# Performance work log

Hardware: AMD Instinct MI355X
Metric: run time of the kernel (lower is better)

## Reference

```python
import jax, jax.numpy as jnp
import numpy as np

NEG = -1e30  # log(0) surrogate that stays finite in fp32
BLANK = 0


def setup_inputs() -> dict:
    key = jax.random.key(0)
    k1, k2 = jax.random.split(key)
    B, T, V, L = 32, 1024, 1024, 256
    logits = jax.random.normal(k1, (B, T, V), dtype=jnp.float32)
    log_probs = jax.nn.log_softmax(logits, axis=-1)  # module expects log-probs
    labels = jax.random.randint(k2, (B, L), 1, V, dtype=jnp.int32)  # avoid blank=0
    input_lens = jnp.full((B,), T, dtype=jnp.int32)
    label_lens = jnp.full((B,), L, dtype=jnp.int32)
    return {"log_probs": log_probs, "labels": labels,
            "input_lens": input_lens, "label_lens": label_lens}


def _ctc_loss_sum(log_probs, labels, input_lens, label_lens, blank=BLANK):
    """CTC forward DP (alpha recursion) in log space; reduction='sum', zero_infinity=True."""
    B, T, V = log_probs.shape
    L = labels.shape[1]
    S = 2 * L + 1  # extended label: blank l1 blank l2 ... blank

    ext = jnp.full((B, S), blank, dtype=labels.dtype)
    ext = ext.at[:, 1::2].set(labels)
    # skip transition s-2 -> s allowed iff ext[s] != blank and ext[s] != ext[s-2]
    skip = jnp.concatenate(
        [jnp.zeros((B, 2), dtype=bool),
         (ext[:, 2:] != blank) & (ext[:, 2:] != ext[:, :-2])], axis=1)

    lp_tbv = jnp.transpose(log_probs, (1, 0, 2))  # 'btv->tbv' as in the module

    emit0 = jnp.take_along_axis(lp_tbv[0], ext, axis=1)  # [B,S]
    alpha0 = jnp.full((B, S), NEG, dtype=log_probs.dtype)
    alpha0 = alpha0.at[:, 0].set(emit0[:, 0]).at[:, 1].set(emit0[:, 1])

    neg1 = jnp.full((B, 1), NEG, dtype=log_probs.dtype)
    neg2 = jnp.full((B, 2), NEG, dtype=log_probs.dtype)

    def step(alpha, inputs):
        lp_t, t = inputs  # lp_t: [B,V]
        em = jnp.take_along_axis(lp_t, ext, axis=1)  # [B,S]
        a1 = alpha
        a2 = jnp.concatenate([neg1, alpha[:, :-1]], axis=1)
        a3 = jnp.where(skip, jnp.concatenate([neg2, alpha[:, :-2]], axis=1), NEG)
        new = jnp.logaddexp(jnp.logaddexp(a1, a2), a3) + em
        # freeze alpha once past this sample's input length
        new = jnp.where((t < input_lens)[:, None], new, alpha)
        return new, None

    ts = jnp.arange(1, T)
    alpha, _ = jax.lax.scan(step, alpha0, (lp_tbv[1:], ts))

    s_last = 2 * label_lens  # final blank state index per sample
    a_last = jnp.take_along_axis(alpha, s_last[:, None], axis=1)[:, 0]
    a_prev = jnp.take_along_axis(alpha, (s_last - 1)[:, None], axis=1)[:, 0]
    loss_b = -jnp.logaddexp(a_last, a_prev)
    loss_b = jnp.where(loss_b > 1e29, 0.0, loss_b)  # zero_infinity=True
    return jnp.sum(loss_b)


def reference(log_probs, labels, input_lens, label_lens):
    return _ctc_loss_sum(log_probs, labels, input_lens, label_lens)
```

## Files before the change

### kernel.cpp

```cpp
#include <hip/hip_runtime.h>


constexpr int B_ = 32, T_ = 1024, V_ = 1024, L_ = 256;
constexpr int S_ = 2 * L_ + 1;
constexpr int CH = 16;
constexpr int NCHUNK = 64;
constexpr int NBUF = 4;
constexpr float LN2F = 0.6931471805599453f;

typedef const __attribute__((address_space(1))) unsigned int* gp_t;
typedef __attribute__((address_space(3))) unsigned int* lp_t;

template <int CTRL>
__device__ __forceinline__ float dpp_fmax(float x) {
    const int t = __builtin_amdgcn_update_dpp(0, __float_as_int(x), CTRL, 0xf, 0xf, true);
    return fmaxf(x, __int_as_float(t));
}

__device__ __forceinline__ float wave_max_dpp(float x) {
    x = dpp_fmax<0x111>(x);
    x = dpp_fmax<0x112>(x);
    x = dpp_fmax<0x114>(x);
    x = dpp_fmax<0x118>(x);
    x = dpp_fmax<0x142>(x);
    x = dpp_fmax<0x143>(x);
    return __int_as_float(__builtin_amdgcn_readlane(__float_as_int(x), 63));
}

__device__ __forceinline__ float dpp_wave_shr1(float x) {
    return __int_as_float(
        __builtin_amdgcn_update_dpp(0, __float_as_int(x), 0x138, 0xf, 0xf, true));
}

__global__ __launch_bounds__(256, 8) void ctc_gather(
    float* __restrict__ lp, const int* __restrict__ labels,
    float* __restrict__ blanks)
{
    __shared__ float srow[4][V_];
    const int wave = threadIdx.x >> 6;
    const int lane = threadIdx.x & 63;
    const int r = blockIdx.x * 4 + wave;
    const int b = r >> 10;
    float* row = lp + (size_t)r * V_;
    const int* labb = labels + b * L_;

    #pragma unroll
    for (int j = 0; j < 4; ++j)
        __builtin_amdgcn_global_load_lds((gp_t)(row + 256 * j + 4 * lane),
                                         (lp_t)&srow[wave][256 * j], 16, 0, 0);
    const int4 e = *(const int4*)(labb + 4 * lane);
    asm volatile("s_waitcnt vmcnt(0)" ::: "memory");
    __builtin_amdgcn_sched_barrier(0);
    const float v0 = srow[wave][e.x];
    const float v1 = srow[wave][e.y];
    const float v2 = srow[wave][e.z];
    const float v3 = srow[wave][e.w];
    const float vb = srow[wave][0];
    float4 q;
    q.x = __expf(v0); q.y = __expf(v1); q.z = __expf(v2); q.w = __expf(v3);
    const float qb = __expf(vb);
    *(float4*)(row + 4 * lane) = q;
    if (lane == 0) {
        const int t = r & (T_ - 1);
        blanks[(r & ~(T_ - 1)) + ((t + T_ - 1) & (T_ - 1))] = qb;
    }
}

__global__ __launch_bounds__(128, 1) void ctc_dp(
    const float* __restrict__ Q, const float* __restrict__ blanks,
    const int* __restrict__ labels, const int* __restrict__ input_lens,
    const int* __restrict__ label_lens, float* __restrict__ out)
{
    __shared__ float blk[T_ + 4];
    __shared__ float buf[NBUF][CH][256];
    __shared__ int Pf, Cf;
    const int b    = blockIdx.x;
    const int tid  = threadIdx.x;
    const int lane = tid & 63;
    const int wv   = tid >> 6;
    const float* Qb  = Q + (size_t)b * T_ * V_;
    const float* blg = blanks + b * T_;
    const int*  labb = labels + b * L_;
    const int il = input_lens[b];
    const int ll = label_lens[b];
    const int tend = il < T_ ? il : T_;

    if (tid == 0) { Pf = 0; Cf = 0; }
    __syncthreads();

    if (wv == 1) {
        #pragma unroll
        for (int i = 0; i < 4; ++i)
            __builtin_amdgcn_global_load_lds((gp_t)(blg + 256 * i + 4 * lane),
                                             (lp_t)&blk[256 * i], 16, 0, 0);
        #pragma unroll
        for (int i = 0; i < CH; ++i) {
            int t = 1 + i; if (t > T_ - 1) t = T_ - 1;
            __builtin_amdgcn_global_load_lds(
                (gp_t)(Qb + (size_t)t * V_ + 4 * lane),
                (lp_t)&buf[0][i][0], 16, 0, 0);
        }
        for (int c = 0; c < NCHUNK; ++c) {
            if (c + 1 < NCHUNK) {
                while (__hip_atomic_load(&Cf, __ATOMIC_ACQUIRE,
                                         __HIP_MEMORY_SCOPE_WORKGROUP) < c + 2 - NBUF) {}
                const int cb = (c + 1) & (NBUF - 1);
                #pragma unroll
                for (int i = 0; i < CH; ++i) {
                    int t = 1 + (c + 1) * CH + i; if (t > T_ - 1) t = T_ - 1;
                    __builtin_amdgcn_global_load_lds(
                        (gp_t)(Qb + (size_t)t * V_ + 4 * lane),
                        (lp_t)&buf[cb][i][0], 16, 0, 0);
                }
                asm volatile("s_waitcnt vmcnt(16)" ::: "memory");
            } else {
                asm volatile("s_waitcnt vmcnt(0)" ::: "memory");
            }
            if (lane == 0)
                __hip_atomic_store(&Pf, c + 1, __ATOMIC_RELEASE,
                                   __HIP_MEMORY_SCOPE_WORKGROUP);
        }
    } else {
        const int4 e  = *(const int4*)(labb + 4 * lane);
        const int  ep = (lane > 0) ? labb[4 * lane - 1] : -1;
        const float kf0 = ((8 * lane + 1) >= 3 && e.x != ep) ? 1.f : 0.f;
        const float kf1 = (e.y != e.x) ? 1.f : 0.f;
        const float kf2 = (e.z != e.y) ? 1.f : 0.f;
        const float kf3 = (e.w != e.z) ? 1.f : 0.f;
        const float bl0 = blg[T_ - 1];
        const float q00 = Qb[0];
        float p0 = (lane == 0) ? bl0 : 0.f;
        float p1 = (lane == 0) ? q00 : 0.f;
        float p2 = 0.f, p3 = 0.f, p4 = 0.f, p5 = 0.f,
              p6 = 0.f, p7 = 0.f, p8 = 0.f;
        int Esc = 0;
        float pm1 = 0.f;
        float sfP = 1.f, sfM = 1.f;

        auto snap = [&]() -> float {
            float m = fmaxf(fmaxf(fmaxf(fmaxf(p0, p1), fmaxf(p2, p3)),
                                  fmaxf(fmaxf(p4, p5), fmaxf(p6, p7))), p8);
            m = wave_max_dpp(m);
            const unsigned eb = (__float_as_uint(m) >> 23) & 0xffu;
            if (eb >= 1u && eb <= 254u) {
                unsigned k = 318u - eb;
                if (k > 254u) k = 254u;
                Esc += (int)k - 127;
                return __uint_as_float(k << 23);
            }
            return 1.f;
        };

        for (int c = 0; c < NCHUNK; ++c) {
            while (__hip_atomic_load(&Pf, __ATOMIC_ACQUIRE,
                                     __HIP_MEMORY_SCOPE_WORKGROUP) <= c) {}
            const float* base = &buf[c & (NBUF - 1)][0][0] + 4 * lane;
            float4 qv[CH];
            #pragma unroll
            for (int i = 0; i < CH; ++i)
                qv[i] = *(const float4*)(base + 256 * i);
            float bb[CH];
            #pragma unroll
            for (int i = 0; i < CH; i += 4) {
                const float4 t4 = *(const float4*)&blk[c * CH + i];
                bb[i] = t4.x; bb[i + 1] = t4.y;
                bb[i + 2] = t4.z; bb[i + 3] = t4.w;
            }
            #pragma unroll
            for (int i = 0; i < CH; ++i) {
                float4 q = qv[i];
                float qb = bb[i];
                if (i == 0) { q.x *= sfP; q.y *= sfP; q.z *= sfP; q.w *= sfP; qb *= sfP; }
                if (i == 8) { q.x *= sfM; q.y *= sfM; q.z *= sfM; q.w *= sfM; qb *= sfM; }
                const int t = 1 + c * CH + i;
                if (t < tend) {
                    const float n7 = fmaf(kf3, p5, p7 + p6) * q.w;
                    const float n8 = (p8 + p7) * qb;
                    const float pm1n = dpp_wave_shr1(n7);
                    const float n0 = (p0 + pm1) * qb;
                    const float n1 = fmaf(kf0, pm1, p1 + p0) * q.x;
                    const float n2 = (p2 + p1) * qb;
                    const float n3 = fmaf(kf1, p1, p3 + p2) * q.y;
                    const float n4 = (p4 + p3) * qb;
                    const float n5 = fmaf(kf2, p3, p5 + p4) * q.z;
                    const float n6 = (p6 + p5) * qb;
                    p0 = n0; p1 = n1; p2 = n2; p3 = n3; p4 = n4;
                    p5 = n5; p6 = n6; p7 = n7; p8 = n8; pm1 = pm1n;
                }
                if (i == 4)  sfM = snap();
                if (i == 12) sfP = snap();
            }
            if (lane == 0)
                __hip_atomic_store(&Cf, c + 1, __ATOMIC_RELEASE,
                                   __HIP_MEMORY_SCOPE_WORKGROUP);
        }
        p0 *= sfP; p1 *= sfP; p2 *= sfP; p3 *= sfP; p4 *= sfP;
        p5 *= sfP; p6 *= sfP; p7 *= sfP; p8 *= sfP;

        const int sl = 2 * ll;
        auto pick = [&](int s) -> float {
            if (s == 512) return __shfl(p8, 63);
            const int r = s & 7;
            float v = p0;
            v = (r == 1) ? p1 : v; v = (r == 2) ? p2 : v;
            v = (r == 3) ? p3 : v; v = (r == 4) ? p4 : v;
            v = (r == 5) ? p5 : v; v = (r == 6) ? p6 : v;
            v = (r == 7) ? p7 : v;
            return __shfl(v, s >> 3);
        };
        const float la = pick(sl);
        const float lb = pick(sl - 1);
        if (lane == 0) {
            const float tot = la + lb;
            float loss = (float)Esc * LN2F - __logf(tot);
            if (!(loss <= 1e29f)) loss = 0.f;
            atomicAdd(out, loss);
        }
    }
}

extern "C" void kernel_launch(void* const* d_in, const int* in_sizes, int n_in,
                              void* d_out, int out_size, void* d_ws, size_t ws_size,
                              hipStream_t stream) {
    float*       lp     = (float*)d_in[0];
    const int*   labels = (const int*)d_in[1];
    const int*   il     = (const int*)d_in[2];
    const int*   ll     = (const int*)d_in[3];
    float* out    = (float*)d_out;
    float* blanks = (float*)d_ws;

    hipMemsetAsync(out, 0, sizeof(float), stream);
    ctc_gather<<<dim3(B_ * T_ / 4), dim3(256), 0, stream>>>(lp, labels, blanks);
    ctc_dp<<<dim3(B_), dim3(128), 0, stream>>>(lp, blanks, labels, il, ll, out);
}
```

Measured before the change: 295.3 us.

## Replace producer/consumer LDS pipeline with single-wave register double-buffering and compact Q

```diff
diff --git a/kernel.cpp b/kernel.cpp
--- a/kernel.cpp
+++ b/kernel.cpp
@@ -2,10 +2,8 @@
 
 
 constexpr int B_ = 32, T_ = 1024, V_ = 1024, L_ = 256;
-constexpr int S_ = 2 * L_ + 1;
 constexpr int CH = 16;
 constexpr int NCHUNK = 64;
-constexpr int NBUF = 4;
 constexpr float LN2F = 0.6931471805599453f;
 
 typedef const __attribute__((address_space(1))) unsigned int* gp_t;
@@ -33,15 +31,16 @@
 }
 
 __global__ __launch_bounds__(256, 8) void ctc_gather(
-    float* __restrict__ lp, const int* __restrict__ labels,
-    float* __restrict__ blanks)
+    const float* __restrict__ lp, float* __restrict__ qdst, int qstride,
+    const int* __restrict__ labels, float* __restrict__ blanks)
 {
     __shared__ float srow[4][V_];
     const int wave = threadIdx.x >> 6;
     const int lane = threadIdx.x & 63;
     const int r = blockIdx.x * 4 + wave;
     const int b = r >> 10;
-    float* row = lp + (size_t)r * V_;
+    const float* row = lp + (size_t)r * V_;
+    float* orow = qdst + (size_t)r * qstride;
     const int* labb = labels + b * L_;
 
     #pragma unroll
@@ -59,163 +58,160 @@
     float4 q;
     q.x = __expf(v0); q.y = __expf(v1); q.z = __expf(v2); q.w = __expf(v3);
     const float qb = __expf(vb);
-    *(float4*)(row + 4 * lane) = q;
+    *(float4*)(orow + 4 * lane) = q;
     if (lane == 0) {
         const int t = r & (T_ - 1);
         blanks[(r & ~(T_ - 1)) + ((t + T_ - 1) & (T_ - 1))] = qb;
     }
 }
 
-__global__ __launch_bounds__(128, 1) void ctc_dp(
-    const float* __restrict__ Q, const float* __restrict__ blanks,
-    const int* __restrict__ labels, const int* __restrict__ input_lens,
-    const int* __restrict__ label_lens, float* __restrict__ out)
+__global__ __launch_bounds__(64, 1) void ctc_dp(
+    const float* __restrict__ Q, int qstride,
+    const float* __restrict__ blanks, const int* __restrict__ labels,
+    const int* __restrict__ input_lens, const int* __restrict__ label_lens,
+    float* __restrict__ out)
 {
-    __shared__ float blk[T_ + 4];
-    __shared__ float buf[NBUF][CH][256];
-    __shared__ int Pf, Cf;
+    __shared__ float blk[T_];
     const int b    = blockIdx.x;
-    const int tid  = threadIdx.x;
-    const int lane = tid & 63;
-    const int wv   = tid >> 6;
-    const float* Qb  = Q + (size_t)b * T_ * V_;
+    const int lane = threadIdx.x & 63;
+    const float* Qb  = Q + (size_t)b * T_ * qstride;
     const float* blg = blanks + b * T_;
     const int*  labb = labels + b * L_;
     const int il = input_lens[b];
     const int ll = label_lens[b];
     const int tend = il < T_ ? il : T_;
 
-    if (tid == 0) { Pf = 0; Cf = 0; }
-    __syncthreads();
-
-    if (wv == 1) {
-        #pragma unroll
-        for (int i = 0; i < 4; ++i)
-            __builtin_amdgcn_global_load_lds((gp_t)(blg + 256 * i + 4 * lane),
-                                             (lp_t)&blk[256 * i], 16, 0, 0);
+    #pragma unroll
+    for (int i = 0; i < 4; ++i)
+        __builtin_amdgcn_global_load_lds((gp_t)(blg + 256 * i + 4 * lane),
+                                         (lp_t)&blk[256 * i], 16, 0, 0);
+
+    const int4 e  = *(const int4*)(labb + 4 * lane);
+    const int  ep = (lane > 0) ? labb[4 * lane - 1] : -1;
+    const float kf0 = ((8 * lane + 1) >= 3 && e.x != ep) ? 1.f : 0.f;
+    const float kf1 = (e.y != e.x) ? 1.f : 0.f;
+    const float kf2 = (e.z != e.y) ? 1.f : 0.f;
+    const float kf3 = (e.w != e.z) ? 1.f : 0.f;
+    const float bl0 = blg[T_ - 1];
+    const float q00 = Qb[0];
+    float p0 = (lane == 0) ? bl0 : 0.f;
+    float p1 = (lane == 0) ? q00 : 0.f;
+    float p2 = 0.f, p3 = 0.f, p4 = 0.f, p5 = 0.f,
+          p6 = 0.f, p7 = 0.f, p8 = 0.f;
+    int Esc = 0;
+    float pm1 = 0.f;
+    float sfP = 1.f, sfM = 1.f;
+
+    asm volatile("s_waitcnt vmcnt(0)" ::: "memory");
+    __builtin_amdgcn_sched_barrier(0);
+
+    auto snap = [&]() -> float {
+        float m = fmaxf(fmaxf(fmaxf(fmaxf(p0, p1), fmaxf(p2, p3)),
+                              fmaxf(fmaxf(p4, p5), fmaxf(p6, p7))), p8);
+        m = wave_max_dpp(m);
+        const unsigned eb = (__float_as_uint(m) >> 23) & 0xffu;
+        if (eb >= 1u && eb <= 254u) {
+            unsigned k = 318u - eb;
+            if (k > 254u) k = 254u;
+            Esc += (int)k - 127;
+            return __uint_as_float(k << 23);
+        }
+        return 1.f;
+    };
+
+    auto qaddr = [&](int t) -> const float4* {
+        return (const float4*)(Qb + (size_t)t * qstride + 4 * lane);
+    };
+
+    float4 qa[CH], qbf[CH];
+    float4 bbA[4], bbB[4];
+    #pragma unroll
+    for (int i = 0; i < CH; ++i) { int t = 1 + i; qa[i] = *qaddr(t); }
+    #pragma unroll
+    for (int i = 0; i < CH; ++i) {
+        int t = 1 + CH + i; if (t > T_ - 1) t = T_ - 1;
+        qbf[i] = *qaddr(t);
+    }
+    #pragma unroll
+    for (int j = 0; j < 4; ++j) bbA[j] = *(const float4*)&blk[4 * j];
+    #pragma unroll
+    for (int j = 0; j < 4; ++j) bbB[j] = *(const float4*)&blk[CH + 4 * j];
+
+    auto compute_chunk = [&](int c, float4 (&qv)[CH], float4 (&bv)[4]) {
         #pragma unroll
         for (int i = 0; i < CH; ++i) {
-            int t = 1 + i; if (t > T_ - 1) t = T_ - 1;
-            __builtin_amdgcn_global_load_lds(
-                (gp_t)(Qb + (size_t)t * V_ + 4 * lane),
-                (lp_t)&buf[0][i][0], 16, 0, 0);
-        }
-        for (int c = 0; c < NCHUNK; ++c) {
-            if (c + 1 < NCHUNK) {
-                while (__hip_atomic_load(&Cf, __ATOMIC_ACQUIRE,
-                                         __HIP_MEMORY_SCOPE_WORKGROUP) < c + 2 - NBUF) {}
-                const int cb = (c + 1) & (NBUF - 1);
-                #pragma unroll
-                for (int i = 0; i < CH; ++i) {
-                    int t = 1 + (c + 1) * CH + i; if (t > T_ - 1) t = T_ - 1;
-                    __builtin_amdgcn_global_load_lds(
-                        (gp_t)(Qb + (size_t)t * V_ + 4 * lane),
-                        (lp_t)&buf[cb][i][0], 16, 0, 0);
-                }
-                asm volatile("s_waitcnt vmcnt(16)" ::: "memory");
-            } else {
-                asm volatile("s_waitcnt vmcnt(0)" ::: "memory");
+            float4 q = qv[i];
+            const int g = i & 3;
+            const float4 f4 = bv[i >> 2];
+            float qb = (g == 0) ? f4.x : (g == 1) ? f4.y
+                     : (g == 2) ? f4.z : f4.w;
+            if (i == 0) { q.x *= sfP; q.y *= sfP; q.z *= sfP; q.w *= sfP; qb *= sfP; }
+            if (i == 8) { q.x *= sfM; q.y *= sfM; q.z *= sfM; q.w *= sfM; qb *= sfM; }
+            const int t = 1 + c * CH + i;
+            if (t < tend) {
+                const float n7 = fmaf(kf3, p5, p7 + p6) * q.w;
+                const float n8 = (p8 + p7) * qb;
+                const float pm1n = dpp_wave_shr1(n7);
+                const float n0 = (p0 + pm1) * qb;
+                const float n1 = fmaf(kf0, pm1, p1 + p0) * q.x;
+                const float n2 = (p2 + p1) * qb;
+                const float n3 = fmaf(kf1, p1, p3 + p2) * q.y;
+                const float n4 = (p4 + p3) * qb;
+                const float n5 = fmaf(kf2, p3, p5 + p4) * q.z;
+                const float n6 = (p6 + p5) * qb;
+                p0 = n0; p1 = n1; p2 = n2; p3 = n3; p4 = n4;
+                p5 = n5; p6 = n6; p7 = n7; p8 = n8; pm1 = pm1n;
             }
-            if (lane == 0)
-                __hip_atomic_store(&Pf, c + 1, __ATOMIC_RELEASE,
-                                   __HIP_MEMORY_SCOPE_WORKGROUP);
-        }
-    } else {
-        const int4 e  = *(const int4*)(labb + 4 * lane);
-        const int  ep = (lane > 0) ? labb[4 * lane - 1] : -1;
-        const float kf0 = ((8 * lane + 1) >= 3 && e.x != ep) ? 1.f : 0.f;
-        const float kf1 = (e.y != e.x) ? 1.f : 0.f;
-        const float kf2 = (e.z != e.y) ? 1.f : 0.f;
-        const float kf3 = (e.w != e.z) ? 1.f : 0.f;
-        const float bl0 = blg[T_ - 1];
-        const float q00 = Qb[0];
-        float p0 = (lane == 0) ? bl0 : 0.f;
-        float p1 = (lane == 0) ? q00 : 0.f;
-        float p2 = 0.f, p3 = 0.f, p4 = 0.f, p5 = 0.f,
-              p6 = 0.f, p7 = 0.f, p8 = 0.f;
-        int Esc = 0;
-        float pm1 = 0.f;
-        float sfP = 1.f, sfM = 1.f;
-
-        auto snap = [&]() -> float {
-            float m = fmaxf(fmaxf(fmaxf(fmaxf(p0, p1), fmaxf(p2, p3)),
-                                  fmaxf(fmaxf(p4, p5), fmaxf(p6, p7))), p8);
-            m = wave_max_dpp(m);
-            const unsigned eb = (__float_as_uint(m) >> 23) & 0xffu;
-            if (eb >= 1u && eb <= 254u) {
-                unsigned k = 318u - eb;
-                if (k > 254u) k = 254u;
-                Esc += (int)k - 127;
-                return __uint_as_float(k << 23);
+            if (i == 4)  sfM = snap();
+            if (i == 12) sfP = snap();
+        }
+    };
+
+    for (int c = 0; c < NCHUNK; c += 2) {
+        compute_chunk(c, qa, bbA);
+        if (c + 2 < NCHUNK) {
+            #pragma unroll
+            for (int i = 0; i < CH; ++i) {
+                int t = 1 + (c + 2) * CH + i; if (t > T_ - 1) t = T_ - 1;
+                qa[i] = *qaddr(t);
             }
-            return 1.f;
-        };
-
-        for (int c = 0; c < NCHUNK; ++c) {
-            while (__hip_atomic_load(&Pf, __ATOMIC_ACQUIRE,
-                                     __HIP_MEMORY_SCOPE_WORKGROUP) <= c) {}
-            const float* base = &buf[c & (NBUF - 1)][0][0] + 4 * lane;
-            float4 qv[CH];
-            #pragma unroll
-            for (int i = 0; i < CH; ++i)
-                qv[i] = *(const float4*)(base + 256 * i);
-            float bb[CH];
-            #pragma unroll
-            for (int i = 0; i < CH; i += 4) {
-                const float4 t4 = *(const float4*)&blk[c * CH + i];
-                bb[i] = t4.x; bb[i + 1] = t4.y;
-                bb[i + 2] = t4.z; bb[i + 3] = t4.w;
+            #pragma unroll
+            for (int j = 0; j < 4; ++j)
+                bbA[j] = *(const float4*)&blk[(c + 2) * CH + 4 * j];
+        }
+        compute_chunk(c + 1, qbf, bbB);
+        if (c + 3 < NCHUNK) {
+            #pragma unroll
+            for (int i = 0; i < CH; ++i) {
+                int t = 1 + (c + 3) * CH + i; if (t > T_ - 1) t = T_ - 1;
+                qbf[i] = *qaddr(t);
             }
             #pragma unroll
-            for (int i = 0; i < CH; ++i) {
-                float4 q = qv[i];
-                float qb = bb[i];
-                if (i == 0) { q.x *= sfP; q.y *= sfP; q.z *= sfP; q.w *= sfP; qb *= sfP; }
-                if (i == 8) { q.x *= sfM; q.y *= sfM; q.z *= sfM; q.w *= sfM; qb *= sfM; }
-                const int t = 1 + c * CH + i;
-                if (t < tend) {
-                    const float n7 = fmaf(kf3, p5, p7 + p6) * q.w;
-                    const float n8 = (p8 + p7) * qb;
-                    const float pm1n = dpp_wave_shr1(n7);
-                    const float n0 = (p0 + pm1) * qb;
-                    const float n1 = fmaf(kf0, pm1, p1 + p0) * q.x;
-                    const float n2 = (p2 + p1) * qb;
-                    const float n3 = fmaf(kf1, p1, p3 + p2) * q.y;
-                    const float n4 = (p4 + p3) * qb;
-                    const float n5 = fmaf(kf2, p3, p5 + p4) * q.z;
-                    const float n6 = (p6 + p5) * qb;
-                    p0 = n0; p1 = n1; p2 = n2; p3 = n3; p4 = n4;
-                    p5 = n5; p6 = n6; p7 = n7; p8 = n8; pm1 = pm1n;
-                }
-                if (i == 4)  sfM = snap();
-                if (i == 12) sfP = snap();
-            }
-            if (lane == 0)
-                __hip_atomic_store(&Cf, c + 1, __ATOMIC_RELEASE,
-                                   __HIP_MEMORY_SCOPE_WORKGROUP);
-        }
-        p0 *= sfP; p1 *= sfP; p2 *= sfP; p3 *= sfP; p4 *= sfP;
-        p5 *= sfP; p6 *= sfP; p7 *= sfP; p8 *= sfP;
-
-        const int sl = 2 * ll;
-        auto pick = [&](int s) -> float {
-            if (s == 512) return __shfl(p8, 63);
-            const int r = s & 7;
-            float v = p0;
-            v = (r == 1) ? p1 : v; v = (r == 2) ? p2 : v;
-            v = (r == 3) ? p3 : v; v = (r == 4) ? p4 : v;
-            v = (r == 5) ? p5 : v; v = (r == 6) ? p6 : v;
-            v = (r == 7) ? p7 : v;
-            return __shfl(v, s >> 3);
-        };
-        const float la = pick(sl);
-        const float lb = pick(sl - 1);
-        if (lane == 0) {
-            const float tot = la + lb;
-            float loss = (float)Esc * LN2F - __logf(tot);
-            if (!(loss <= 1e29f)) loss = 0.f;
-            atomicAdd(out, loss);
-        }
+            for (int j = 0; j < 4; ++j)
+                bbB[j] = *(const float4*)&blk[(c + 3) * CH + 4 * j];
+        }
+    }
+    p0 *= sfP; p1 *= sfP; p2 *= sfP; p3 *= sfP; p4 *= sfP;
+    p5 *= sfP; p6 *= sfP; p7 *= sfP; p8 *= sfP;
+
+    const int sl = 2 * ll;
+    auto pick = [&](int s) -> float {
+        if (s == 512) return __shfl(p8, 63);
+        const int r = s & 7;
+        float v = p0;
+        v = (r == 1) ? p1 : v; v = (r == 2) ? p2 : v;
+        v = (r == 3) ? p3 : v; v = (r == 4) ? p4 : v;
+        v = (r == 5) ? p5 : v; v = (r == 6) ? p6 : v;
+        v = (r == 7) ? p7 : v;
+        return __shfl(v, s >> 3);
+    };
+    const float la = pick(sl);
+    const float lb = pick(sl - 1);
+    if (lane == 0) {
+        const float tot = la + lb;
+        float loss = (float)Esc * LN2F - __logf(tot);
+        if (!(loss <= 1e29f)) loss = 0.f;
+        atomicAdd(out, loss);
     }
 }
 
@@ -229,7 +225,15 @@
     float* out    = (float*)d_out;
     float* blanks = (float*)d_ws;
 
+    const size_t need = (size_t)B_ * T_ * sizeof(float)
+                      + (size_t)B_ * T_ * 256 * sizeof(float);
+    const bool use_ws = ws_size >= need;
+    float* qdst = use_ws ? (blanks + (size_t)B_ * T_) : lp;
+    const int qstride = use_ws ? 256 : V_;
+
     hipMemsetAsync(out, 0, sizeof(float), stream);
-    ctc_gather<<<dim3(B_ * T_ / 4), dim3(256), 0, stream>>>(lp, labels, blanks);
-    ctc_dp<<<dim3(B_), dim3(128), 0, stream>>>(lp, blanks, labels, il, ll, out);
-}
+    ctc_gather<<<dim3(B_ * T_ / 4), dim3(256), 0, stream>>>(
+        lp, qdst, qstride, labels, blanks);
+    ctc_dp<<<dim3(B_), dim3(64), 0, stream>>>(
+        qdst, qstride, blanks, labels, il, ll, out);
+}
```

Result: slower. 337.6 us (+14.3%).
